# Kernel tuning notes

Measured on AMD Instinct MI355X. Metric: run time of the kernel, lower is better.

## Reference

```python
import jax, jax.numpy as jnp
import numpy as np

N_ATOMS = 50000
N_EDGES = 1_600_000
FEAT = 128
FP_LEN = 2048
RADIUS = 3


def setup_inputs() -> dict:
    key = jax.random.key(0)
    k = jax.random.split(key, 6)
    atomsFeatures = jax.random.normal(k[0], (N_ATOMS, FEAT), dtype=jnp.float32)
    W1 = jax.random.normal(k[1], (FEAT, FEAT), dtype=jnp.float32) * 0.05
    b1 = jnp.zeros((FEAT,), dtype=jnp.float32)
    W2 = jax.random.normal(k[2], (FEAT, FP_LEN), dtype=jnp.float32) * 0.05
    b2 = jnp.zeros((FP_LEN,), dtype=jnp.float32)
    edge_src = jax.random.randint(k[3], (N_EDGES,), 0, N_ATOMS, dtype=jnp.int32)
    edge_dst = jax.random.randint(k[4], (N_EDGES,), 0, N_ATOMS, dtype=jnp.int32)
    return {"atomsFeatures": atomsFeatures, "W1": W1, "b1": b1,
            "W2": W2, "b2": b2, "edge_src": edge_src, "edge_dst": edge_dst}


def reference(atomsFeatures, W1, b1, W2, b2, edge_src, edge_dst):
    # Duvenaud-style neural fingerprint:
    # per radius step: x_i <- x_i + sum_{j in N(i)} x_j ; h = relu(lin1(x));
    # fp += sum_atoms softmax(lin2(h)); x <- h
    fp0 = jnp.zeros((1, FP_LEN), dtype=atomsFeatures.dtype)

    def step(carry, _):
        x, fp = carry
        # neighbor-sum via segment reduce over the edge list (self + neighbors)
        agg = x + jax.ops.segment_sum(x[edge_src], edge_dst, num_segments=N_ATOMS)
        h = jax.nn.relu(agg @ W1 + b1)            # [N, FEAT]
        probs = jax.nn.softmax(h @ W2 + b2, axis=1)  # [N, FP_LEN]
        fp = fp + jnp.sum(probs, axis=0, keepdims=True)
        return (h, fp), None

    (_, fp), _ = jax.lax.scan(step, (atomsFeatures, fp0), None, length=RADIUS)
    return fp
```

## Files before the change

### kernel.cpp

```cpp
#include <hip/hip_runtime.h>

typedef short short8 __attribute__((ext_vector_type(8)));
typedef __bf16 bf16x8 __attribute__((ext_vector_type(8)));
typedef float f32x4 __attribute__((ext_vector_type(4)));
typedef unsigned long long u64;

#define FEAT 128
#define FPL 2048
#define LOG2E 1.4426950408889634f

__device__ __forceinline__ float b2f(unsigned int u) {
  union { unsigned int u; float f; } c; c.u = u << 16; return c.f;
}
__device__ __forceinline__ unsigned short f2b(float f) {
  union { float f; unsigned int u; } c; c.f = f;
  unsigned int r = c.u + 0x7fffu + ((c.u >> 16) & 1u);
  return (unsigned short)(r >> 16);
}
__device__ __forceinline__ f32x4 mfma16(short8 a, short8 b, f32x4 c) {
  return __builtin_amdgcn_mfma_f32_16x16x32_bf16(
      __builtin_bit_cast(bf16x8, a), __builtin_bit_cast(bf16x8, b), c, 0, 0, 0);
}
__device__ __forceinline__ float exp2x(float x) {
  float r; asm("v_exp_f32 %0, %1" : "=v"(r) : "v"(x)); return r;
}
__device__ __forceinline__ void add8(float* a, ulonglong2 v) {
  u64 lo = v.x, hi = v.y;
  a[0] += b2f((unsigned int)(lo & 0xffffu));
  a[1] += b2f((unsigned int)((lo >> 16) & 0xffffu));
  a[2] += b2f((unsigned int)((lo >> 32) & 0xffffu));
  a[3] += b2f((unsigned int)(lo >> 48));
  a[4] += b2f((unsigned int)(hi & 0xffffu));
  a[5] += b2f((unsigned int)((hi >> 16) & 0xffffu));
  a[6] += b2f((unsigned int)((hi >> 32) & 0xffffu));
  a[7] += b2f((unsigned int)(hi >> 48));
}

__global__ void cvt_kernel(const float* __restrict__ in, unsigned short* __restrict__ out, int n2) {
  int i = blockIdx.x * 256 + threadIdx.x;
  if (i < n2) {
    float2 v = ((const float2*)in)[i];
    unsigned int lo = f2b(v.x), hi = f2b(v.y);
    ((unsigned int*)out)[i] = lo | (hi << 16);
  }
}

__global__ void cvtT_kernel(const float* __restrict__ W, unsigned short* __restrict__ WT,
                            int K, int N, float scale) {
  int i = blockIdx.x * 256 + threadIdx.x;
  if (i < K * N) {
    int k = i / N, c = i - k * N;
    WT[(size_t)c * K + k] = f2b(W[i] * scale);
  }
}

__global__ void countrank_kernel(const int* __restrict__ dst, int* __restrict__ cnt,
                                 int* __restrict__ rank, int n) {
  int i = blockIdx.x * 256 + threadIdx.x;
  if (i < n) rank[i] = atomicAdd(&cnt[dst[i]], 1);
}

__global__ __launch_bounds__(1024) void scan1_kernel(const int* __restrict__ cnt,
    int* __restrict__ ex, int* __restrict__ chunkSum, int n) {
  __shared__ int sd[1024];
  const int i = blockIdx.x * 1024 + threadIdx.x;
  int v = (i < n) ? cnt[i] : 0;
  sd[threadIdx.x] = v;
  __syncthreads();
  int sum = v;
  for (int off = 1; off < 1024; off <<= 1) {
    int t = (threadIdx.x >= (unsigned)off) ? sd[threadIdx.x - off] : 0;
    __syncthreads();
    sum += t;
    sd[threadIdx.x] = sum;
    __syncthreads();
  }
  if (i < n) ex[i] = sum - v;
  if (threadIdx.x == 1023) chunkSum[blockIdx.x] = sum;
}

__global__ __launch_bounds__(1024) void scan2_kernel(const int* __restrict__ chunkSum,
    int* __restrict__ chunkOff, int nChunks) {
  __shared__ int sd[1024];
  int v = (threadIdx.x < (unsigned)nChunks) ? chunkSum[threadIdx.x] : 0;
  sd[threadIdx.x] = v;
  __syncthreads();
  int sum = v;
  for (int off = 1; off < 1024; off <<= 1) {
    int t = (threadIdx.x >= (unsigned)off) ? sd[threadIdx.x - off] : 0;
    __syncthreads();
    sum += t;
    sd[threadIdx.x] = sum;
    __syncthreads();
  }
  if (threadIdx.x < (unsigned)nChunks) chunkOff[threadIdx.x] = sum - v;
}

__global__ void scan3_kernel(const int* __restrict__ ex, const int* __restrict__ chunkOff,
    const int* __restrict__ chunkSum, int* __restrict__ rp, int n, int nChunks) {
  int i = blockIdx.x * 256 + threadIdx.x;
  if (i < n) rp[i] = ex[i] + chunkOff[i >> 10];
  if (i == 0) rp[n] = chunkOff[nChunks - 1] + chunkSum[nChunks - 1];
}

__global__ __launch_bounds__(256) void fillp_kernel(const int* __restrict__ src,
    const int* __restrict__ dst, const int* __restrict__ rank,
    const int* __restrict__ rp, int* __restrict__ col, int n, int nAtoms) {
  const int part = blockIdx.x & 3;
  const int blkInPart = blockIdx.x >> 2;
  const int nBlkPerPart = gridDim.x >> 2;
  const int partSize = (nAtoms + 3) >> 2;
  const int lo = part * partSize;
  const int hi = min(lo + partSize, nAtoms);
  const int stride = nBlkPerPart * 256;
  for (int i = blkInPart * 256 + (int)threadIdx.x; i < n; i += stride) {
    int d = __builtin_nontemporal_load(&dst[i]);
    if (d >= lo && d < hi) {
      col[rp[d] + rank[i]] = src[i];
    }
  }
}

__global__ __launch_bounds__(256) void gather_kernel(const unsigned short* __restrict__ x,
    const int* __restrict__ rp, const int* __restrict__ col,
    unsigned short* __restrict__ agg, int n) {
  int wid = (blockIdx.x * 256 + threadIdx.x) >> 6;
  int lane = threadIdx.x & 63;
  if (wid >= n) return;
  const int q = lane >> 4;
  const int l16 = lane & 15;
  const ulonglong2* xv = (const ulonglong2*)x;

  float a[8];
#pragma unroll
  for (int k = 0; k < 8; ++k) a[k] = 0.f;
  if (q == 0) add8(a, xv[(size_t)wid * 16 + l16]);

  const int beg = rp[wid], end = rp[wid + 1];
  int j = beg;
  for (; j + 8 <= end; j += 8) {
    int c0 = col[j + q];
    int c1 = col[j + 4 + q];
    ulonglong2 v0 = xv[(size_t)c0 * 16 + l16];
    ulonglong2 v1 = xv[(size_t)c1 * 16 + l16];
    add8(a, v0);
    add8(a, v1);
  }
  if (j + 4 <= end) {
    int c = col[j + q];
    add8(a, xv[(size_t)c * 16 + l16]);
    j += 4;
  }
  if (j + q < end) {
    int c = col[j + q];
    add8(a, xv[(size_t)c * 16 + l16]);
  }
#pragma unroll
  for (int k = 0; k < 8; ++k) {
    a[k] += __shfl_xor(a[k], 16, 64);
    a[k] += __shfl_xor(a[k], 32, 64);
  }
  if (q == 0) {
    ulonglong2 r;
    r.x = (u64)f2b(a[0]) | ((u64)f2b(a[1]) << 16) | ((u64)f2b(a[2]) << 32) | ((u64)f2b(a[3]) << 48);
    r.y = (u64)f2b(a[4]) | ((u64)f2b(a[5]) << 16) | ((u64)f2b(a[6]) << 32) | ((u64)f2b(a[7]) << 48);
    ((ulonglong2*)agg)[(size_t)wid * 16 + l16] = r;
  }
}

__global__ __launch_bounds__(256) void gemm1_kernel(
    const unsigned short* __restrict__ A, const unsigned short* __restrict__ W1T,
    const float* __restrict__ b1, unsigned short* __restrict__ H, int n) {
  const int wave = threadIdx.x >> 6;
  const int lane = threadIdx.x & 63;
  const int lr = lane & 15, lg = lane >> 4;
  const int rowBase = blockIdx.x * 64 + wave * 16;
  short8 a[4];
#pragma unroll
  for (int kt = 0; kt < 4; ++kt)
    a[kt] = *(const short8*)(A + (size_t)(rowBase + lr) * FEAT + kt * 32 + lg * 8);
  f32x4 acc[8];
#pragma unroll
  for (int ct = 0; ct < 8; ++ct) {
    const unsigned short* bp = W1T + (size_t)(ct * 16 + lr) * FEAT + lg * 8;
    f32x4 c = {0.f, 0.f, 0.f, 0.f};
    c = mfma16(a[0], *(const short8*)(bp), c);
    c = mfma16(a[1], *(const short8*)(bp + 32), c);
    c = mfma16(a[2], *(const short8*)(bp + 64), c);
    c = mfma16(a[3], *(const short8*)(bp + 96), c);
    acc[ct] = c;
  }
#pragma unroll
  for (int ct = 0; ct < 8; ++ct) {
    const int c = ct * 16 + lr;
    const float bias = b1[c];
#pragma unroll
    for (int j = 0; j < 4; ++j) {
      const int row = rowBase + lg * 4 + j;
      if (row < n) {
        float v = acc[ct][j] + bias;
        H[(size_t)row * FEAT + c] = f2b(v > 0.f ? v : 0.f);
      }
    }
  }
}


__global__ __launch_bounds__(512) void statT_kernel(
    const unsigned short* __restrict__ H, const unsigned short* __restrict__ W2T,
    const float* __restrict__ b2, float* __restrict__ pm, float* __restrict__ ps,
    int nPad) {
  __shared__ short8 ldsB[2048];
  __shared__ float ldsBias[128];
  const int wave = threadIdx.x >> 6;
  const int lane = threadIdx.x & 63;
  const int lr = lane & 15, lg = lane >> 4;
  const int nRowBlk = nPad >> 8;
  const int rowBlk = blockIdx.x % nRowBlk;
  const int colBlk = blockIdx.x / nRowBlk;
  const int rowBase = rowBlk * 256 + wave * 32;
  const int colBase = colBlk * 128;

#pragma unroll
  for (int r = 0; r < 4; ++r) {
    const int p = r * 8 + wave;
    const int ct = p >> 2, q = p & 3;
    ldsB[p * 64 + lane] =
        *(const short8*)(W2T + (size_t)(colBase + ct * 16 + lr) * FEAT + (q * 4 + lg) * 8);
  }
  if (threadIdx.x < 128) ldsBias[threadIdx.x] = b2[colBase + threadIdx.x] * LOG2E;

  short8 a[2][4];
#pragma unroll
  for (int g = 0; g < 2; ++g)
#pragma unroll
    for (int kt = 0; kt < 4; ++kt)
      a[g][kt] = *(const short8*)(H + (size_t)(rowBase + g * 16 + lr) * FEAT + kt * 32 + lg * 8);
  __syncthreads();

  float m[2][4], s[2][4];
#pragma unroll
  for (int g = 0; g < 2; ++g)
#pragma unroll
    for (int j = 0; j < 4; ++j) { m[g][j] = -1e30f; s[g][j] = 0.f; }

#pragma unroll 4
  for (int ct = 0; ct < 8; ++ct) {
    short8 q0 = ldsB[(ct * 4 + 0) * 64 + lane];
    short8 q1 = ldsB[(ct * 4 + 1) * 64 + lane];
    short8 q2 = ldsB[(ct * 4 + 2) * 64 + lane];
    short8 q3 = ldsB[(ct * 4 + 3) * 64 + lane];
    f32x4 c0 = {0.f, 0.f, 0.f, 0.f};
    f32x4 c1 = {0.f, 0.f, 0.f, 0.f};
    c0 = mfma16(a[0][0], q0, c0);
    c1 = mfma16(a[1][0], q0, c1);
    c0 = mfma16(a[0][1], q1, c0);
    c1 = mfma16(a[1][1], q1, c1);
    c0 = mfma16(a[0][2], q2, c0);
    c1 = mfma16(a[1][2], q2, c1);
    c0 = mfma16(a[0][3], q3, c0);
    c1 = mfma16(a[1][3], q3, c1);
    const float bs = ldsBias[ct * 16 + lr];
    float d0[4], d1[4];
#pragma unroll
    for (int j = 0; j < 4; ++j) {
      d0[j] = c0[j] + bs - m[0][j];
      d1[j] = c1[j] + bs - m[1][j];
    }
    float dmax = fmaxf(fmaxf(fmaxf(d0[0], d0[1]), fmaxf(d0[2], d0[3])),
                       fmaxf(fmaxf(d1[0], d1[1]), fmaxf(d1[2], d1[3])));
    if (__any(dmax > 12.f)) {
#pragma unroll
      for (int j = 0; j < 4; ++j) {
        float e0 = d0[j] + m[0][j], e1 = d1[j] + m[1][j];
        float nm0 = fmaxf(m[0][j], e0);
        s[0][j] = s[0][j] * exp2x(m[0][j] - nm0) + exp2x(e0 - nm0);
        m[0][j] = nm0;
        float nm1 = fmaxf(m[1][j], e1);
        s[1][j] = s[1][j] * exp2x(m[1][j] - nm1) + exp2x(e1 - nm1);
        m[1][j] = nm1;
      }
    } else {
#pragma unroll
      for (int j = 0; j < 4; ++j) {
        s[0][j] += exp2x(d0[j]);
        s[1][j] += exp2x(d1[j]);
      }
    }
  }
#pragma unroll
  for (int g = 0; g < 2; ++g)
#pragma unroll
    for (int j = 0; j < 4; ++j) {
#pragma unroll
      for (int d = 1; d < 16; d <<= 1) {
        float om = __shfl_xor(m[g][j], d, 64);
        float os = __shfl_xor(s[g][j], d, 64);
        float nm = fmaxf(m[g][j], om);
        s[g][j] = s[g][j] * exp2x(m[g][j] - nm) + os * exp2x(om - nm);
        m[g][j] = nm;
      }
    }
  if (lr == 0) {
#pragma unroll
    for (int g = 0; g < 2; ++g)
#pragma unroll
      for (int j = 0; j < 4; ++j) {
        const int row = rowBase + g * 16 + lg * 4 + j;
        pm[(size_t)colBlk * nPad + row] = m[g][j];
        ps[(size_t)colBlk * nPad + row] = s[g][j];
      }
  }
}

__global__ void mergeT_kernel(const float* __restrict__ pm, const float* __restrict__ ps,
                              float* __restrict__ T, int nPad) {
  int r = blockIdx.x * 256 + threadIdx.x;
  if (r < nPad) {
    float M = pm[r];
#pragma unroll
    for (int k = 1; k < 16; ++k) M = fmaxf(M, pm[(size_t)k * nPad + r]);
    float S = 0.f;
#pragma unroll
    for (int k = 0; k < 16; ++k) S += ps[(size_t)k * nPad + r] * exp2x(pm[(size_t)k * nPad + r] - M);
    T[r] = M + __log2f(S);
  }
}

__global__ __launch_bounds__(512) void fpacc_kernel(
    const unsigned short* __restrict__ H, const unsigned short* __restrict__ W2T,
    const float* __restrict__ b2, const float* __restrict__ T,
    float* __restrict__ partials, int n, int nPad) {
  __shared__ short8 ldsB[2048];
  __shared__ float ldsBias[128];
  __shared__ float fp_w[8][128];
  const int wave = threadIdx.x >> 6;
  const int lane = threadIdx.x & 63;
  const int lr = lane & 15, lg = lane >> 4;
  const int nRowBlk = nPad >> 8;
  const int rowBlk = blockIdx.x % nRowBlk;
  const int colBlk = blockIdx.x / nRowBlk;
  const int rowBase = rowBlk * 256 + wave * 32;
  const int colBase = colBlk * 128;

#pragma unroll
  for (int r = 0; r < 4; ++r) {
    const int p = r * 8 + wave;
    const int ct = p >> 2, q = p & 3;
    ldsB[p * 64 + lane] =
        *(const short8*)(W2T + (size_t)(colBase + ct * 16 + lr) * FEAT + (q * 4 + lg) * 8);
  }
  if (threadIdx.x < 128) ldsBias[threadIdx.x] = b2[colBase + threadIdx.x] * LOG2E;

  short8 a[2][4];
#pragma unroll
  for (int g = 0; g < 2; ++g)
#pragma unroll
    for (int kt = 0; kt < 4; ++kt)
      a[g][kt] = *(const short8*)(H + (size_t)(rowBase + g * 16 + lr) * FEAT + kt * 32 + lg * 8);
  float Tq[2][4];
#pragma unroll
  for (int g = 0; g < 2; ++g)
#pragma unroll
    for (int j = 0; j < 4; ++j) {
      const int row = rowBase + g * 16 + lg * 4 + j;
      Tq[g][j] = (row < n) ? T[row] : 1e30f;
    }
  __syncthreads();

#pragma unroll 4
  for (int ct = 0; ct < 8; ++ct) {
    short8 q0 = ldsB[(ct * 4 + 0) * 64 + lane];
    short8 q1 = ldsB[(ct * 4 + 1) * 64 + lane];
    short8 q2 = ldsB[(ct * 4 + 2) * 64 + lane];
    short8 q3 = ldsB[(ct * 4 + 3) * 64 + lane];
    f32x4 c0 = {0.f, 0.f, 0.f, 0.f};
    f32x4 c1 = {0.f, 0.f, 0.f, 0.f};
    c0 = mfma16(a[0][0], q0, c0);
    c1 = mfma16(a[1][0], q0, c1);
    c0 = mfma16(a[0][1], q1, c0);
    c1 = mfma16(a[1][1], q1, c1);
    c0 = mfma16(a[0][2], q2, c0);
    c1 = mfma16(a[1][2], q2, c1);
    c0 = mfma16(a[0][3], q3, c0);
    c1 = mfma16(a[1][3], q3, c1);
    const float bs = ldsBias[ct * 16 + lr];
    float p = exp2x(c0[0] + (bs - Tq[0][0])) + exp2x(c0[1] + (bs - Tq[0][1])) +
              exp2x(c0[2] + (bs - Tq[0][2])) + exp2x(c0[3] + (bs - Tq[0][3])) +
              exp2x(c1[0] + (bs - Tq[1][0])) + exp2x(c1[1] + (bs - Tq[1][1])) +
              exp2x(c1[2] + (bs - Tq[1][2])) + exp2x(c1[3] + (bs - Tq[1][3]));
    p += __shfl_xor(p, 16, 64);
    p += __shfl_xor(p, 32, 64);
    if (lg == 0) fp_w[wave][ct * 16 + lr] = p;
  }
  __syncthreads();
  if (threadIdx.x < 128) {
    float sum = 0.f;
#pragma unroll
    for (int w = 0; w < 8; ++w) sum += fp_w[w][threadIdx.x];
    partials[(size_t)rowBlk * FPL + colBase + threadIdx.x] += sum;
  }
}

__global__ void reduce_kernel(const float* __restrict__ partials, float* __restrict__ out, int nPart) {
  int c = blockIdx.x * 256 + threadIdx.x;
  if (c < FPL) {
    float s = 0.f;
    for (int p = 0; p < nPart; ++p) s += partials[(size_t)p * FPL + c];
    out[c] = s;
  }
}

extern "C" void kernel_launch(void* const* d_in, const int* in_sizes, int n_in,
                              void* d_out, int out_size, void* d_ws, size_t ws_size,
                              hipStream_t stream) {
  const float* atoms = (const float*)d_in[0];
  const float* W1 = (const float*)d_in[1];
  const float* b1 = (const float*)d_in[2];
  const float* W2 = (const float*)d_in[3];
  const float* b2 = (const float*)d_in[4];
  const int* esrc = (const int*)d_in[5];
  const int* edst = (const int*)d_in[6];
  const int nAtoms = in_sizes[0] / FEAT;
  const int nEdges = in_sizes[5];
  if (nAtoms <= 0) return;

  const int g2Blocks = (nAtoms + 255) / 256;
  const int nPad = g2Blocks * 256;
  const int g1Blocks = nPad / 64;
  const int nChunks = (nAtoms + 1023) / 1024;

  size_t off = 0;
  auto alloc = [&](size_t bytes) -> void* {
    void* p = (char*)d_ws + off;
    off += (bytes + 255) & ~(size_t)255;
    return p;
  };
  unsigned short* P = (unsigned short*)alloc((size_t)nPad * FEAT * 2);
  unsigned short* Q = (unsigned short*)alloc((size_t)nPad * FEAT * 2);
  unsigned short* W1T = (unsigned short*)alloc((size_t)FEAT * FEAT * 2);
  unsigned short* W2T = (unsigned short*)alloc((size_t)FEAT * FPL * 2);
  int* counts = (int*)alloc((size_t)nAtoms * 4);
  int* rank = (int*)alloc((size_t)nEdges * 4);
  int* rp = (int*)alloc(((size_t)nAtoms + 1) * 4);
  int* ex = (int*)alloc((size_t)nAtoms * 4);
  int* chunkSum = (int*)alloc((size_t)nChunks * 4);
  int* chunkOff = (int*)alloc((size_t)nChunks * 4);
  int* col = (int*)alloc((size_t)nEdges * 4);
  float* pm = (float*)alloc((size_t)16 * nPad * 4);
  float* ps = (float*)alloc((size_t)16 * nPad * 4);
  float* Trow = (float*)alloc((size_t)nPad * 4);
  float* partials = (float*)alloc((size_t)g2Blocks * FPL * 4);

  hipMemsetAsync(counts, 0, (size_t)nAtoms * 4, stream);
  hipMemsetAsync(partials, 0, (size_t)g2Blocks * FPL * 4, stream);
  hipMemsetAsync(P + (size_t)nAtoms * FEAT, 0, (size_t)(nPad - nAtoms) * FEAT * 2, stream);
  hipMemsetAsync(Q + (size_t)nAtoms * FEAT, 0, (size_t)(nPad - nAtoms) * FEAT * 2, stream);

  const int n2 = in_sizes[0] / 2;
  cvt_kernel<<<(n2 + 255) / 256, 256, 0, stream>>>(atoms, P, n2);
  cvtT_kernel<<<(FEAT * FEAT + 255) / 256, 256, 0, stream>>>(W1, W1T, FEAT, FEAT, 1.0f);
  cvtT_kernel<<<(FEAT * FPL + 255) / 256, 256, 0, stream>>>(W2, W2T, FEAT, FPL, LOG2E);
  countrank_kernel<<<(nEdges + 255) / 256, 256, 0, stream>>>(edst, counts, rank, nEdges);
  scan1_kernel<<<nChunks, 1024, 0, stream>>>(counts, ex, chunkSum, nAtoms);
  scan2_kernel<<<1, 1024, 0, stream>>>(chunkSum, chunkOff, nChunks);
  scan3_kernel<<<(nAtoms + 255) / 256, 256, 0, stream>>>(ex, chunkOff, chunkSum, rp, nAtoms, nChunks);
  fillp_kernel<<<1024, 256, 0, stream>>>(esrc, edst, rank, rp, col, nEdges, nAtoms);

  unsigned short* x = P;
  unsigned short* y = Q;
  for (int step = 0; step < 3; ++step) {
    gather_kernel<<<(nAtoms + 3) / 4, 256, 0, stream>>>(x, rp, col, y, nAtoms);
    gemm1_kernel<<<g1Blocks, 256, 0, stream>>>(y, W1T, b1, y, nAtoms);
    statT_kernel<<<g2Blocks * 16, 512, 0, stream>>>(y, W2T, b2, pm, ps, nPad);
    mergeT_kernel<<<(nPad + 255) / 256, 256, 0, stream>>>(pm, ps, Trow, nPad);
    fpacc_kernel<<<g2Blocks * 16, 512, 0, stream>>>(y, W2T, b2, Trow, partials, nAtoms, nPad);
    unsigned short* t = x; x = y; y = t;
  }
  reduce_kernel<<<(FPL + 255) / 256, 256, 0, stream>>>(partials, (float*)d_out, g2Blocks);
}
```

Before: 707.8 us.

## Widen softmax column tiles to 512 per block and batch countrank atomics

The statT and fpacc kernels now each cover 512 output columns per block by looping over four 128-column W2 sub-tiles. The H row fragments stay in registers across those sub-tiles, so each block does four times the work and the partial-stat buffers shrink from 16 to 4 column splits. This cuts repeated H loads and lowers the block count and mergeT traffic, at the cost of extra barriers inside blocks, serialized W2 tile loads, and LDS atomics in fpacc. Separately, countrank now handles 8 edges per thread so several atomics can be in flight per thread.

```diff
diff --git a/kernel.cpp b/kernel.cpp
--- a/kernel.cpp
+++ b/kernel.cpp
@@ -56,8 +56,19 @@
 
 __global__ void countrank_kernel(const int* __restrict__ dst, int* __restrict__ cnt,
                                  int* __restrict__ rank, int n) {
-  int i = blockIdx.x * 256 + threadIdx.x;
-  if (i < n) rank[i] = atomicAdd(&cnt[dst[i]], 1);
+  const int base = (blockIdx.x * 256 + (int)threadIdx.x) * 8;
+  if (base + 8 <= n) {
+    int d[8];
+#pragma unroll
+    for (int k = 0; k < 8; ++k) d[k] = dst[base + k];
+    int r[8];
+#pragma unroll
+    for (int k = 0; k < 8; ++k) r[k] = atomicAdd(&cnt[d[k]], 1);
+#pragma unroll
+    for (int k = 0; k < 8; ++k) rank[base + k] = r[k];
+  } else {
+    for (int i = base; i < n; ++i) rank[i] = atomicAdd(&cnt[dst[i]], 1);
+  }
 }
 
 __global__ __launch_bounds__(1024) void scan1_kernel(const int* __restrict__ cnt,
@@ -219,16 +230,6 @@
   const int rowBlk = blockIdx.x % nRowBlk;
   const int colBlk = blockIdx.x / nRowBlk;
   const int rowBase = rowBlk * 256 + wave * 32;
-  const int colBase = colBlk * 128;
-
-#pragma unroll
-  for (int r = 0; r < 4; ++r) {
-    const int p = r * 8 + wave;
-    const int ct = p >> 2, q = p & 3;
-    ldsB[p * 64 + lane] =
-        *(const short8*)(W2T + (size_t)(colBase + ct * 16 + lr) * FEAT + (q * 4 + lg) * 8);
-  }
-  if (threadIdx.x < 128) ldsBias[threadIdx.x] = b2[colBase + threadIdx.x] * LOG2E;
 
   short8 a[2][4];
 #pragma unroll
@@ -236,7 +237,6 @@
 #pragma unroll
     for (int kt = 0; kt < 4; ++kt)
       a[g][kt] = *(const short8*)(H + (size_t)(rowBase + g * 16 + lr) * FEAT + kt * 32 + lg * 8);
-  __syncthreads();
 
   float m[2][4], s[2][4];
 #pragma unroll
@@ -244,47 +244,61 @@
 #pragma unroll
     for (int j = 0; j < 4; ++j) { m[g][j] = -1e30f; s[g][j] = 0.f; }
 
+  for (int cb = 0; cb < 4; ++cb) {
+    const int colBase = colBlk * 512 + cb * 128;
+    if (cb) __syncthreads();
+#pragma unroll
+    for (int r = 0; r < 4; ++r) {
+      const int p = r * 8 + wave;
+      const int ct = p >> 2, q = p & 3;
+      ldsB[p * 64 + lane] =
+          *(const short8*)(W2T + (size_t)(colBase + ct * 16 + lr) * FEAT + (q * 4 + lg) * 8);
+    }
+    if (threadIdx.x < 128) ldsBias[threadIdx.x] = b2[colBase + threadIdx.x] * LOG2E;
+    __syncthreads();
+
 #pragma unroll 4
-  for (int ct = 0; ct < 8; ++ct) {
-    short8 q0 = ldsB[(ct * 4 + 0) * 64 + lane];
-    short8 q1 = ldsB[(ct * 4 + 1) * 64 + lane];
-    short8 q2 = ldsB[(ct * 4 + 2) * 64 + lane];
-    short8 q3 = ldsB[(ct * 4 + 3) * 64 + lane];
-    f32x4 c0 = {0.f, 0.f, 0.f, 0.f};
-    f32x4 c1 = {0.f, 0.f, 0.f, 0.f};
-    c0 = mfma16(a[0][0], q0, c0);
-    c1 = mfma16(a[1][0], q0, c1);
-    c0 = mfma16(a[0][1], q1, c0);
-    c1 = mfma16(a[1][1], q1, c1);
-    c0 = mfma16(a[0][2], q2, c0);
-    c1 = mfma16(a[1][2], q2, c1);
-    c0 = mfma16(a[0][3], q3, c0);
-    c1 = mfma16(a[1][3], q3, c1);
-    const float bs = ldsBias[ct * 16 + lr];
-    float d0[4], d1[4];
-#pragma unroll
-    for (int j = 0; j < 4; ++j) {
-      d0[j] = c0[j] + bs - m[0][j];
-      d1[j] = c1[j] + bs - m[1][j];
-    }
-    float dmax = fmaxf(fmaxf(fmaxf(d0[0], d0[1]), fmaxf(d0[2], d0[3])),
-                       fmaxf(fmaxf(d1[0], d1[1]), fmaxf(d1[2], d1[3])));
-    if (__any(dmax > 12.f)) {
+    for (int ct = 0; ct < 8; ++ct) {
+      short8 q0 = ldsB[(ct * 4 + 0) * 64 + lane];
+      short8 q1 = ldsB[(ct * 4 + 1) * 64 + lane];
+      short8 q2 = ldsB[(ct * 4 + 2) * 64 + lane];
+      short8 q3 = ldsB[(ct * 4 + 3) * 64 + lane];
+      f32x4 c0 = {0.f, 0.f, 0.f, 0.f};
+      f32x4 c1 = {0.f, 0.f, 0.f, 0.f};
+      c0 = mfma16(a[0][0], q0, c0);
+      c1 = mfma16(a[1][0], q0, c1);
+      c0 = mfma16(a[0][1], q1, c0);
+      c1 = mfma16(a[1][1], q1, c1);
+      c0 = mfma16(a[0][2], q2, c0);
+      c1 = mfma16(a[1][2], q2, c1);
+      c0 = mfma16(a[0][3], q3, c0);
+      c1 = mfma16(a[1][3], q3, c1);
+      const float bs = ldsBias[ct * 16 + lr];
+      float d0[4], d1[4];
 #pragma unroll
       for (int j = 0; j < 4; ++j) {
-        float e0 = d0[j] + m[0][j], e1 = d1[j] + m[1][j];
-        float nm0 = fmaxf(m[0][j], e0);
-        s[0][j] = s[0][j] * exp2x(m[0][j] - nm0) + exp2x(e0 - nm0);
-        m[0][j] = nm0;
-        float nm1 = fmaxf(m[1][j], e1);
-        s[1][j] = s[1][j] * exp2x(m[1][j] - nm1) + exp2x(e1 - nm1);
-        m[1][j] = nm1;
+        d0[j] = c0[j] + bs - m[0][j];
+        d1[j] = c1[j] + bs - m[1][j];
       }
-    } else {
-#pragma unroll
-      for (int j = 0; j < 4; ++j) {
-        s[0][j] += exp2x(d0[j]);
-        s[1][j] += exp2x(d1[j]);
+      float dmax = fmaxf(fmaxf(fmaxf(d0[0], d0[1]), fmaxf(d0[2], d0[3])),
+                         fmaxf(fmaxf(d1[0], d1[1]), fmaxf(d1[2], d1[3])));
+      if (__any(dmax > 12.f)) {
+#pragma unroll
+        for (int j = 0; j < 4; ++j) {
+          float e0 = d0[j] + m[0][j], e1 = d1[j] + m[1][j];
+          float nm0 = fmaxf(m[0][j], e0);
+          s[0][j] = s[0][j] * exp2x(m[0][j] - nm0) + exp2x(e0 - nm0);
+          m[0][j] = nm0;
+          float nm1 = fmaxf(m[1][j], e1);
+          s[1][j] = s[1][j] * exp2x(m[1][j] - nm1) + exp2x(e1 - nm1);
+          m[1][j] = nm1;
+        }
+      } else {
+#pragma unroll
+        for (int j = 0; j < 4; ++j) {
+          s[0][j] += exp2x(d0[j]);
+          s[1][j] += exp2x(d1[j]);
+        }
       }
     }
   }
@@ -319,10 +333,10 @@
   if (r < nPad) {
     float M = pm[r];
 #pragma unroll
-    for (int k = 1; k < 16; ++k) M = fmaxf(M, pm[(size_t)k * nPad + r]);
+    for (int k = 1; k < 4; ++k) M = fmaxf(M, pm[(size_t)k * nPad + r]);
     float S = 0.f;
 #pragma unroll
-    for (int k = 0; k < 16; ++k) S += ps[(size_t)k * nPad + r] * exp2x(pm[(size_t)k * nPad + r] - M);
+    for (int k = 0; k < 4; ++k) S += ps[(size_t)k * nPad + r] * exp2x(pm[(size_t)k * nPad + r] - M);
     T[r] = M + __log2f(S);
   }
 }
@@ -333,7 +347,7 @@
     float* __restrict__ partials, int n, int nPad) {
   __shared__ short8 ldsB[2048];
   __shared__ float ldsBias[128];
-  __shared__ float fp_w[8][128];
+  __shared__ float fp_lds[512];
   const int wave = threadIdx.x >> 6;
   const int lane = threadIdx.x & 63;
   const int lr = lane & 15, lg = lane >> 4;
@@ -341,16 +355,7 @@
   const int rowBlk = blockIdx.x % nRowBlk;
   const int colBlk = blockIdx.x / nRowBlk;
   const int rowBase = rowBlk * 256 + wave * 32;
-  const int colBase = colBlk * 128;
-
-#pragma unroll
-  for (int r = 0; r < 4; ++r) {
-    const int p = r * 8 + wave;
-    const int ct = p >> 2, q = p & 3;
-    ldsB[p * 64 + lane] =
-        *(const short8*)(W2T + (size_t)(colBase + ct * 16 + lr) * FEAT + (q * 4 + lg) * 8);
-  }
-  if (threadIdx.x < 128) ldsBias[threadIdx.x] = b2[colBase + threadIdx.x] * LOG2E;
+  fp_lds[threadIdx.x] = 0.f;
 
   short8 a[2][4];
 #pragma unroll
@@ -366,40 +371,48 @@
       const int row = rowBase + g * 16 + lg * 4 + j;
       Tq[g][j] = (row < n) ? T[row] : 1e30f;
     }
+
+  for (int cb = 0; cb < 4; ++cb) {
+    const int colBase = colBlk * 512 + cb * 128;
+    if (cb) __syncthreads();
+#pragma unroll
+    for (int r = 0; r < 4; ++r) {
+      const int p = r * 8 + wave;
+      const int ct = p >> 2, q = p & 3;
+      ldsB[p * 64 + lane] =
+          *(const short8*)(W2T + (size_t)(colBase + ct * 16 + lr) * FEAT + (q * 4 + lg) * 8);
+    }
+    if (threadIdx.x < 128) ldsBias[threadIdx.x] = b2[colBase + threadIdx.x] * LOG2E;
+    __syncthreads();
+
+#pragma unroll 4
+    for (int ct = 0; ct < 8; ++ct) {
+      short8 q0 = ldsB[(ct * 4 + 0) * 64 + lane];
+      short8 q1 = ldsB[(ct * 4 + 1) * 64 + lane];
+      short8 q2 = ldsB[(ct * 4 + 2) * 64 + lane];
+      short8 q3 = ldsB[(ct * 4 + 3) * 64 + lane];
+      f32x4 c0 = {0.f, 0.f, 0.f, 0.f};
+      f32x4 c1 = {0.f, 0.f, 0.f, 0.f};
+      c0 = mfma16(a[0][0], q0, c0);
+      c1 = mfma16(a[1][0], q0, c1);
+      c0 = mfma16(a[0][1], q1, c0);
+      c1 = mfma16(a[1][1], q1, c1);
+      c0 = mfma16(a[0][2], q2, c0);
+      c1 = mfma16(a[1][2], q2, c1);
+      c0 = mfma16(a[0][3], q3, c0);
+      c1 = mfma16(a[1][3], q3, c1);
+      const float bs = ldsBias[ct * 16 + lr];
+      float p = exp2x(c0[0] + (bs - Tq[0][0])) + exp2x(c0[1] + (bs - Tq[0][1])) +
+                exp2x(c0[2] + (bs - Tq[0][2])) + exp2x(c0[3] + (bs - Tq[0][3])) +
+                exp2x(c1[0] + (bs - Tq[1][0])) + exp2x(c1[1] + (bs - Tq[1][1])) +
+                exp2x(c1[2] + (bs - Tq[1][2])) + exp2x(c1[3] + (bs - Tq[1][3]));
+      p += __shfl_xor(p, 16, 64);
+      p += __shfl_xor(p, 32, 64);
+      if (lg == 0) atomicAdd(&fp_lds[cb * 128 + ct * 16 + lr], p);
+    }
+  }
   __syncthreads();
-
-#pragma unroll 4
-  for (int ct = 0; ct < 8; ++ct) {
-    short8 q0 = ldsB[(ct * 4 + 0) * 64 + lane];
-    short8 q1 = ldsB[(ct * 4 + 1) * 64 + lane];
-    short8 q2 = ldsB[(ct * 4 + 2) * 64 + lane];
-    short8 q3 = ldsB[(ct * 4 + 3) * 64 + lane];
-    f32x4 c0 = {0.f, 0.f, 0.f, 0.f};
-    f32x4 c1 = {0.f, 0.f, 0.f, 0.f};
-    c0 = mfma16(a[0][0], q0, c0);
-    c1 = mfma16(a[1][0], q0, c1);
-    c0 = mfma16(a[0][1], q1, c0);
-    c1 = mfma16(a[1][1], q1, c1);
-    c0 = mfma16(a[0][2], q2, c0);
-    c1 = mfma16(a[1][2], q2, c1);
-    c0 = mfma16(a[0][3], q3, c0);
-    c1 = mfma16(a[1][3], q3, c1);
-    const float bs = ldsBias[ct * 16 + lr];
-    float p = exp2x(c0[0] + (bs - Tq[0][0])) + exp2x(c0[1] + (bs - Tq[0][1])) +
-              exp2x(c0[2] + (bs - Tq[0][2])) + exp2x(c0[3] + (bs - Tq[0][3])) +
-              exp2x(c1[0] + (bs - Tq[1][0])) + exp2x(c1[1] + (bs - Tq[1][1])) +
-              exp2x(c1[2] + (bs - Tq[1][2])) + exp2x(c1[3] + (bs - Tq[1][3]));
-    p += __shfl_xor(p, 16, 64);
-    p += __shfl_xor(p, 32, 64);
-    if (lg == 0) fp_w[wave][ct * 16 + lr] = p;
-  }
-  __syncthreads();
-  if (threadIdx.x < 128) {
-    float sum = 0.f;
-#pragma unroll
-    for (int w = 0; w < 8; ++w) sum += fp_w[w][threadIdx.x];
-    partials[(size_t)rowBlk * FPL + colBase + threadIdx.x] += sum;
-  }
+  partials[(size_t)rowBlk * FPL + colBlk * 512 + threadIdx.x] += fp_lds[threadIdx.x];
 }
 
 __global__ void reduce_kernel(const float* __restrict__ partials, float* __restrict__ out, int nPart) {
@@ -447,8 +460,8 @@
   int* chunkSum = (int*)alloc((size_t)nChunks * 4);
   int* chunkOff = (int*)alloc((size_t)nChunks * 4);
   int* col = (int*)alloc((size_t)nEdges * 4);
-  float* pm = (float*)alloc((size_t)16 * nPad * 4);
-  float* ps = (float*)alloc((size_t)16 * nPad * 4);
+  float* pm = (float*)alloc((size_t)4 * nPad * 4);
+  float* ps = (float*)alloc((size_t)4 * nPad * 4);
   float* Trow = (float*)alloc((size_t)nPad * 4);
   float* partials = (float*)alloc((size_t)g2Blocks * FPL * 4);
 
@@ -461,7 +474,7 @@
   cvt_kernel<<<(n2 + 255) / 256, 256, 0, stream>>>(atoms, P, n2);
   cvtT_kernel<<<(FEAT * FEAT + 255) / 256, 256, 0, stream>>>(W1, W1T, FEAT, FEAT, 1.0f);
   cvtT_kernel<<<(FEAT * FPL + 255) / 256, 256, 0, stream>>>(W2, W2T, FEAT, FPL, LOG2E);
-  countrank_kernel<<<(nEdges + 255) / 256, 256, 0, stream>>>(edst, counts, rank, nEdges);
+  countrank_kernel<<<(nEdges + 2047) / 2048, 256, 0, stream>>>(edst, counts, rank, nEdges);
   scan1_kernel<<<nChunks, 1024, 0, stream>>>(counts, ex, chunkSum, nAtoms);
   scan2_kernel<<<1, 1024, 0, stream>>>(chunkSum, chunkOff, nChunks);
   scan3_kernel<<<(nAtoms + 255) / 256, 256, 0, stream>>>(ex, chunkOff, chunkSum, rp, nAtoms, nChunks);
@@ -472,9 +485,9 @@
   for (int step = 0; step < 3; ++step) {
     gather_kernel<<<(nAtoms + 3) / 4, 256, 0, stream>>>(x, rp, col, y, nAtoms);
     gemm1_kernel<<<g1Blocks, 256, 0, stream>>>(y, W1T, b1, y, nAtoms);
-    statT_kernel<<<g2Blocks * 16, 512, 0, stream>>>(y, W2T, b2, pm, ps, nPad);
+    statT_kernel<<<g2Blocks * 4, 512, 0, stream>>>(y, W2T, b2, pm, ps, nPad);
     mergeT_kernel<<<(nPad + 255) / 256, 256, 0, stream>>>(pm, ps, Trow, nPad);
-    fpacc_kernel<<<g2Blocks * 16, 512, 0, stream>>>(y, W2T, b2, Trow, partials, nAtoms, nPad);
+    fpacc_kernel<<<g2Blocks * 4, 512, 0, stream>>>(y, W2T, b2, Trow, partials, nAtoms, nPad);
     unsigned short* t = x; x = y; y = t;
   }
   reduce_kernel<<<(FPL + 255) / 256, 256, 0, stream>>>(partials, (float*)d_out, g2Blocks);
```

Measured after the change: 757.0 us. 6.9% more time.
